# Optimization experiments

Measured on AMD Instinct MI355X. Metric: run time of the kernel, lower is better.

Reference implementation:

```python
import jax, jax.numpy as jnp
import numpy as np

NUM_EMBEDDINGS = 1024
EMBEDDING_DIM = 64
COMMITMENT_COST = 0.25
N_TOKENS = 131072


def setup_inputs() -> dict:
    key = jax.random.key(0)
    k_in, k_emb = jax.random.split(key)
    inputs = jax.random.normal(k_in, (N_TOKENS, EMBEDDING_DIM), dtype=jnp.float32)
    # torch init: uniform(-1/K, 1/K)
    codebook = jax.random.uniform(
        k_emb, (NUM_EMBEDDINGS, EMBEDDING_DIM), dtype=jnp.float32,
        minval=-1.0 / NUM_EMBEDDINGS, maxval=1.0 / NUM_EMBEDDINGS)
    return {"inputs": inputs, "codebook": codebook}


def reference(inputs, codebook):
    sg = jax.lax.stop_gradient
    distances = (jnp.sum(inputs * inputs, axis=1, keepdims=True)
                 - 2.0 * jnp.matmul(inputs, codebook.T)
                 + jnp.sum(codebook * codebook, axis=1)[None, :])
    encoding_indices = jnp.argmin(distances, axis=1)          # [N]
    # direct gather (same math as one-hot @ codebook)
    quantized = jnp.take(codebook, encoding_indices, axis=0)  # [N, D]
    # original computes e_latent_loss and q_latent_loss identically
    # (both mse(inputs, quantized.detach())), so loss = (1 + beta) * mse
    mse = jnp.mean((sg(quantized) - inputs) ** 2)
    loss = mse + COMMITMENT_COST * mse
    # straight-through estimator
    quantized_st = inputs + sg(quantized - inputs)
    # perplexity from code usage histogram (== mean of one-hot encodings)
    counts = jax.ops.segment_sum(
        jnp.ones((inputs.shape[0],), dtype=jnp.float32),
        encoding_indices, num_segments=NUM_EMBEDDINGS)
    avg_probs = counts / inputs.shape[0]
    perplexity = jnp.exp(-jnp.sum(avg_probs * jnp.log(avg_probs + 1e-10)))
    return loss, quantized_st, perplexity, encoding_indices[:, None]
```

## Files before the change

kernel.cpp:

```cpp
#include <hip/hip_runtime.h>
#include <math.h>

#define NTOK 131072
#define KC   1024
#define DIMV 64
#define NWAVE 16
#define TPW  32
#define TPB  (NWAVE * TPW)
#define CMAX 128
#define EPS  2e-3f

#define OUT_LOSS 0
#define OUT_Q    1
#define OUT_PERP (1 + NTOK * DIMV)
#define OUT_IDX  (2 + NTOK * DIMV)

#define WS_HIST 1
#define WS_NORM 1025
#define WS_PACK_BYTES 12288
#define WS_NEED (WS_PACK_BYTES + KC * DIMV * 2)

typedef __attribute__((ext_vector_type(8))) short short8;
typedef __attribute__((ext_vector_type(4))) float f32x4;

__device__ __forceinline__ float sumsq64_np(const float v[DIMV]) {
#pragma clang fp contract(off)
  {
    float r[8];
#pragma unroll
    for (int j = 0; j < 8; ++j) r[j] = v[j] * v[j];
#pragma unroll
    for (int i = 8; i < 64; i += 8) {
#pragma unroll
      for (int j = 0; j < 8; ++j) r[j] += v[i + j] * v[i + j];
    }
    return ((r[0] + r[1]) + (r[2] + r[3])) + ((r[4] + r[5]) + (r[6] + r[7]));
  }
}

__device__ __forceinline__ unsigned short bf16rne(float f) {
  unsigned int u = __float_as_uint(f);
  return (unsigned short)((u + 0x7fffu + ((u >> 16) & 1u)) >> 16);
}

__global__ void __launch_bounds__(256)
vq_pack_kernel(const float* __restrict__ cb, float* __restrict__ ws) {
  const int e = blockIdx.x * 256 + threadIdx.x;
  const int tile = e >> 7, f = (e >> 6) & 1, l = e & 63;
  const int code = tile * 16 + (l & 15);
  const int kb = f * 32 + (l >> 4) * 8;
  const float4* src = reinterpret_cast<const float4*>(cb + code * DIMV + kb);
  float4 v0 = src[0], v1 = src[1];
  float v[8] = {v0.x, v0.y, v0.z, v0.w, v1.x, v1.y, v1.z, v1.w};
  unsigned int hw[4];
#pragma unroll
  for (int j = 0; j < 4; ++j) {
    hw[j] = (unsigned int)bf16rne(v[2 * j]) |
            ((unsigned int)bf16rne(v[2 * j + 1]) << 16);
  }
  char* pack = (char*)ws + WS_PACK_BYTES;
  *(uint4*)(pack + tile * 2048 + f * 1024 + l * 16) =
      make_uint4(hw[0], hw[1], hw[2], hw[3]);
  if (e < KC) {
    float row[DIMV];
    const float4* r4 = reinterpret_cast<const float4*>(cb + e * DIMV);
#pragma unroll
    for (int i = 0; i < 16; ++i) {
      float4 t = r4[i];
      row[4 * i + 0] = t.x; row[4 * i + 1] = t.y;
      row[4 * i + 2] = t.z; row[4 * i + 3] = t.w;
    }
    ws[WS_NORM + e] = sumsq64_np(row);
  }
}

__global__ void __launch_bounds__(1024, 4)
vq_main_mfma(const float* __restrict__ xin, const float* __restrict__ cb,
             float* __restrict__ out, float* __restrict__ ws) {
  __shared__ __align__(16) char s_pack[131072];
  __shared__ float s_norm[KC];
  __shared__ unsigned int s_hist[KC];
  __shared__ unsigned int s_cand[NWAVE][CMAX];
  __shared__ unsigned long long s_key[NWAVE][TPW];
  __shared__ int s_cnt[NWAVE];

  const int tid = threadIdx.x;
  const int l   = tid & 63;
  const int wv  = tid >> 6;
  const int cls = l & 15;
  const int g   = l >> 4;
  const int blk = blockIdx.x;
  const int tb  = blk * TPB + wv * TPW;

  float* ws_mse = ws;
  unsigned int* ws_hist = (unsigned int*)ws + WS_HIST;
  const float* ws_norm = ws + WS_NORM;
  const char* pack = (const char*)ws + WS_PACK_BYTES;

  {
    const uint4* src = (const uint4*)pack;
    uint4* dst = (uint4*)s_pack;
#pragma unroll
    for (int i = 0; i < 8; ++i) dst[tid + i * 1024] = src[tid + i * 1024];
  }
  s_norm[tid] = ws_norm[tid];
  s_hist[tid] = 0u;
  if (tid < NWAVE * TPW) s_key[tid >> 5][tid & 31] = ~0ull;
  if (tid < NWAVE) s_cnt[tid] = 0;
  __syncthreads();

  short8 af[2][2];
#pragma unroll
  for (int grp = 0; grp < 2; ++grp) {
    const float* xr = xin + (size_t)(tb + grp * 16 + cls) * DIMV + g * 8;
#pragma unroll
    for (int kc = 0; kc < 2; ++kc) {
      float4 v0 = *(const float4*)(xr + kc * 32);
      float4 v1 = *(const float4*)(xr + kc * 32 + 4);
      float vv[8] = {v0.x, v0.y, v0.z, v0.w, v1.x, v1.y, v1.z, v1.w};
#pragma unroll
      for (int j = 0; j < 8; ++j) af[grp][kc][j] = (short)bf16rne(vv[j]);
    }
  }

  float minv[2][4];
#pragma unroll
  for (int grp = 0; grp < 2; ++grp)
#pragma unroll
    for (int j = 0; j < 4; ++j) minv[grp][j] = INFINITY;

#pragma unroll 1
  for (int t = 0; t < 64; ++t) {
    const char* bp = s_pack + t * 2048;
    short8 b0 = *(const short8*)(bp + l * 16);
    short8 b1 = *(const short8*)(bp + 1024 + l * 16);
    float nr = s_norm[t * 16 + cls];
#pragma unroll
    for (int grp = 0; grp < 2; ++grp) {
      f32x4 acc = {0.0f, 0.0f, 0.0f, 0.0f};
      acc = __builtin_amdgcn_mfma_f32_16x16x32_bf16(af[grp][0], b0, acc, 0, 0, 0);
      acc = __builtin_amdgcn_mfma_f32_16x16x32_bf16(af[grp][1], b1, acc, 0, 0, 0);
#pragma unroll
      for (int j = 0; j < 4; ++j)
        minv[grp][j] = fminf(minv[grp][j], fmaf(-2.0f, acc[j], nr));
    }
  }
#pragma unroll
  for (int mask = 1; mask < 16; mask <<= 1) {
#pragma unroll
    for (int grp = 0; grp < 2; ++grp)
#pragma unroll
      for (int j = 0; j < 4; ++j)
        minv[grp][j] = fminf(minv[grp][j], __shfl_xor(minv[grp][j], mask, 64));
  }
  float thr[2][4];
#pragma unroll
  for (int grp = 0; grp < 2; ++grp)
#pragma unroll
    for (int j = 0; j < 4; ++j) thr[grp][j] = minv[grp][j] + EPS;

#pragma unroll 1
  for (int t = 0; t < 64; ++t) {
    const char* bp = s_pack + t * 2048;
    short8 b0 = *(const short8*)(bp + l * 16);
    short8 b1 = *(const short8*)(bp + 1024 + l * 16);
    float nr = s_norm[t * 16 + cls];
#pragma unroll
    for (int grp = 0; grp < 2; ++grp) {
      f32x4 acc = {0.0f, 0.0f, 0.0f, 0.0f};
      acc = __builtin_amdgcn_mfma_f32_16x16x32_bf16(af[grp][0], b0, acc, 0, 0, 0);
      acc = __builtin_amdgcn_mfma_f32_16x16x32_bf16(af[grp][1], b1, acc, 0, 0, 0);
#pragma unroll
      for (int j = 0; j < 4; ++j) {
        float sv = fmaf(-2.0f, acc[j], nr);
        if (sv <= thr[grp][j]) {
          int pos = atomicAdd(&s_cnt[wv], 1);
          if (pos < CMAX)
            s_cand[wv][pos] =
                ((unsigned int)(grp * 16 + g * 4 + j) << 10) |
                (unsigned int)(t * 16 + cls);
        }
      }
    }
  }
  asm volatile("s_waitcnt lgkmcnt(0)" ::: "memory");
  const int cnt = s_cnt[wv];
  int n = cnt < CMAX ? cnt : CMAX;

  for (int base = 0; base < n; base += 64) {
    int i = base + l;
    if (i < n) {
      unsigned int pk = s_cand[wv][i];
      int m = (int)(pk >> 10), k = (int)(pk & 1023);
      const float4* xr4 = (const float4*)(xin + (size_t)(tb + m) * DIMV);
      const float4* er4 = (const float4*)(cb + (size_t)k * DIMV);
      float r[8];
      float dot = 0.0f;
#pragma unroll
      for (int s = 0; s < 8; ++s) {
        float4 a = xr4[2 * s], b = xr4[2 * s + 1];
        float4 ea = er4[2 * s], eb = er4[2 * s + 1];
        float xv[8] = {a.x, a.y, a.z, a.w, b.x, b.y, b.z, b.w};
        float ev[8] = {ea.x, ea.y, ea.z, ea.w, eb.x, eb.y, eb.z, eb.w};
        {
#pragma clang fp contract(off)
#pragma unroll
          for (int j = 0; j < 8; ++j) {
            float sq = xv[j] * xv[j];
            r[j] = (s == 0) ? sq : (r[j] + sq);
          }
        }
#pragma unroll
        for (int j = 0; j < 8; ++j) dot = __builtin_fmaf(ev[j], xv[j], dot);
      }
      float xx = ((r[0] + r[1]) + (r[2] + r[3])) + ((r[4] + r[5]) + (r[6] + r[7]));
      float d = (xx - 2.0f * dot) + s_norm[k];
      unsigned long long key =
          ((unsigned long long)__float_as_uint(d) << 10) | (unsigned long long)k;
      atomicMin(&s_key[wv][m], key);
    }
  }

  if (cnt > CMAX) {
    if (l < TPW) {
      const int m = l;
      float xv[DIMV];
      const float4* xr4 = (const float4*)(xin + (size_t)(tb + m) * DIMV);
#pragma unroll
      for (int i = 0; i < 16; ++i) {
        float4 t4 = xr4[i];
        xv[4 * i + 0] = t4.x; xv[4 * i + 1] = t4.y;
        xv[4 * i + 2] = t4.z; xv[4 * i + 3] = t4.w;
      }
      float xx = sumsq64_np(xv);
      float bd = INFINITY; int bk = 0;
      for (int k = 0; k < KC; ++k) {
        const float* e = cb + (size_t)k * DIMV;
        float dot = 0.0f;
#pragma unroll
        for (int i = 0; i < DIMV; ++i) dot = __builtin_fmaf(e[i], xv[i], dot);
        float d = (xx - 2.0f * dot) + s_norm[k];
        if (d < bd) { bd = d; bk = k; }
      }
      s_key[wv][m] =
          ((unsigned long long)__float_as_uint(bd) << 10) | (unsigned long long)bk;
    }
  }
  asm volatile("s_waitcnt lgkmcnt(0)" ::: "memory");

  {
    const int m = l & 31, h = l >> 5;
    const int token = tb + m;
    unsigned long long key = s_key[wv][m];
    const int bk = (int)(key & 1023ull);
    if (h == 0) {
      out[OUT_IDX + token] = (float)bk;
      atomicAdd(&s_hist[bk], 1u);
    }
    const float4* q4 = (const float4*)(cb + (size_t)bk * DIMV + h * 32);
    const float4* x4 = (const float4*)(xin + (size_t)token * DIMV + h * 32);
    float* oq = out + OUT_Q + (size_t)token * DIMV + h * 32;
    float mse_part = 0.0f;
#pragma unroll
    for (int rr = 0; rr < 8; ++rr) {
      float4 qv = q4[rr], xv = x4[rr];
      float d0 = qv.x - xv.x, d1 = qv.y - xv.y;
      float d2 = qv.z - xv.z, d3 = qv.w - xv.w;
      float4 o;
      o.x = xv.x + d0; o.y = xv.y + d1; o.z = xv.z + d2; o.w = xv.w + d3;
      mse_part = __builtin_fmaf(d0, d0, mse_part);
      mse_part = __builtin_fmaf(d1, d1, mse_part);
      mse_part = __builtin_fmaf(d2, d2, mse_part);
      mse_part = __builtin_fmaf(d3, d3, mse_part);
      *(float4*)(oq + 4 * rr) = o;
    }
#pragma unroll
    for (int mask = 1; mask < 64; mask <<= 1)
      mse_part += __shfl_xor(mse_part, mask, 64);
    if (l == 0) atomicAdd(ws_mse, mse_part);
  }

  __syncthreads();
  {
    unsigned int c = s_hist[tid];
    if (c) atomicAdd(&ws_hist[tid], c);
  }
}

__global__ void __launch_bounds__(256)
vq_main_valu(const float* __restrict__ xin, const float* __restrict__ cb,
             float* __restrict__ out, float* __restrict__ ws) {
  __shared__ float s_norm[KC];
  __shared__ unsigned int s_hist[KC];
  __shared__ float s_cd[256];
  __shared__ int   s_ci[256];
  const int tid = threadIdx.x;
  const int lane = tid & 63;
  const int wv = __builtin_amdgcn_readfirstlane(tid >> 6);
  float* ws_mse = ws;
  unsigned int* ws_hist = (unsigned int*)ws + WS_HIST;

  for (int k = tid; k < KC; k += 256) {
    float e[DIMV];
    const float4* e4 = reinterpret_cast<const float4*>(cb + k * DIMV);
#pragma unroll
    for (int i = 0; i < 16; ++i) {
      float4 t = e4[i];
      e[4 * i + 0] = t.x; e[4 * i + 1] = t.y;
      e[4 * i + 2] = t.z; e[4 * i + 3] = t.w;
    }
    s_norm[k] = sumsq64_np(e);
    s_hist[k] = 0u;
  }
  __syncthreads();

  const int token = blockIdx.x * 64 + lane;
  float x[DIMV];
  const float4* x4 = reinterpret_cast<const float4*>(xin + (long)token * DIMV);
#pragma unroll
  for (int i = 0; i < 16; ++i) {
    float4 t = x4[i];
    x[4 * i + 0] = t.x; x[4 * i + 1] = t.y;
    x[4 * i + 2] = t.z; x[4 * i + 3] = t.w;
  }
  float xx = sumsq64_np(x);

  float best = INFINITY;
  int bidx = 0;
#pragma unroll 1
  for (int kk = 0; kk < KC / 4; ++kk) {
    const int k = wv * (KC / 4) + kk;
    const float* e = cb + k * DIMV;
    float dot = 0.0f;
#pragma unroll
    for (int i = 0; i < DIMV; ++i) dot = __builtin_fmaf(e[i], x[i], dot);
    float d = (xx - 2.0f * dot) + s_norm[k];
    if (d < best) { best = d; bidx = k; }
  }
  s_cd[tid] = best;
  s_ci[tid] = bidx;
  __syncthreads();

  if (wv == 0) {
    float bd = s_cd[lane];
    int   bi = s_ci[lane];
#pragma unroll
    for (int w = 1; w < 4; ++w) {
      float dw = s_cd[w * 64 + lane];
      int   iw = s_ci[w * 64 + lane];
      if (dw < bd) { bd = dw; bi = iw; }
    }
    out[OUT_IDX + token] = (float)bi;
    atomicAdd(&s_hist[bi], 1u);
    const float4* q4 = (const float4*)(cb + (long)bi * DIMV);
    float acc = 0.0f;
    float4* oq4 = reinterpret_cast<float4*>(out + OUT_Q + (long)token * DIMV);
#pragma unroll
    for (int i = 0; i < 16; ++i) {
      float4 qv = q4[i];
      float d0 = qv.x - x[4 * i + 0];
      float d1 = qv.y - x[4 * i + 1];
      float d2 = qv.z - x[4 * i + 2];
      float d3 = qv.w - x[4 * i + 3];
      float4 o;
      o.x = x[4 * i + 0] + d0; o.y = x[4 * i + 1] + d1;
      o.z = x[4 * i + 2] + d2; o.w = x[4 * i + 3] + d3;
      acc = __builtin_fmaf(d0, d0, acc);
      acc = __builtin_fmaf(d1, d1, acc);
      acc = __builtin_fmaf(d2, d2, acc);
      acc = __builtin_fmaf(d3, d3, acc);
      oq4[i] = o;
    }
#pragma unroll
    for (int off = 32; off > 0; off >>= 1) acc += __shfl_down(acc, off, 64);
    if (lane == 0) atomicAdd(ws_mse, acc);
  }
  __syncthreads();
  for (int k = tid; k < KC; k += 256) {
    unsigned int c = s_hist[k];
    if (c) atomicAdd(&ws_hist[k], c);
  }
}

__global__ void __launch_bounds__(1024)
vq_final_kernel(const unsigned int* __restrict__ ws_hist,
                const float* __restrict__ ws_mse,
                float* __restrict__ out) {
  __shared__ float s_red[1024];
  const int t = threadIdx.x;
  float p = (float)ws_hist[t] / 131072.0f;
  float term = p * logf(p + 1e-10f);
  s_red[t] = term;
  __syncthreads();
#pragma unroll
  for (int s = 512; s > 0; s >>= 1) {
    if (t < s) s_red[t] += s_red[t + s];
    __syncthreads();
  }
  if (t == 0) {
    out[OUT_PERP] = expf(-s_red[0]);
    float mse = ws_mse[0] / 8388608.0f;
    out[OUT_LOSS] = mse + 0.25f * mse;
  }
}

extern "C" void kernel_launch(void* const* d_in, const int* in_sizes, int n_in,
                              void* d_out, int out_size, void* d_ws, size_t ws_size,
                              hipStream_t stream) {
  (void)in_sizes; (void)n_in; (void)out_size;
  const float* xin = (const float*)d_in[0];
  const float* cb  = (const float*)d_in[1];
  float* out = (float*)d_out;
  float* ws  = (float*)d_ws;

  hipMemsetAsync(d_ws, 0, sizeof(float) * (1 + KC), stream);
  if (ws_size >= (size_t)(WS_NEED + 256)) {
    hipLaunchKernelGGL(vq_pack_kernel, dim3(32), dim3(256), 0, stream, cb, ws);
    hipLaunchKernelGGL(vq_main_mfma, dim3(NTOK / TPB), dim3(1024), 0, stream,
                       xin, cb, out, ws);
  } else {
    hipLaunchKernelGGL(vq_main_valu, dim3(NTOK / 64), dim3(256), 0, stream,
                       xin, cb, out, ws);
  }
  hipLaunchKernelGGL(vq_final_kernel, dim3(1), dim3(1024), 0, stream,
                     (const unsigned int*)ws + WS_HIST, ws, out);
}
```

Before: 179.5 us.

## Fuse pack, main and final kernels into one MFMA kernel with last-block reduction

Merges the codebook pack, main search and final perplexity kernels into a single kernel. Each block now converts the codebook to bf16 and computes the norms directly into LDS, and the last block to finish (found with an atomic ticket) computes perplexity and loss. Block size drops to 512 threads with 64 tokens per wave (four MFMA row groups). The norm is folded into the accumulator's initial value, the B fragments are software-prefetched, and the refinement epsilon is halved. This removes two launches and the workspace round trip, at the cost of every block redundantly packing the codebook from global memory.

```diff
diff --git a/kernel.cpp b/kernel.cpp
--- a/kernel.cpp
+++ b/kernel.cpp
@@ -4,22 +4,17 @@
 #define NTOK 131072
 #define KC   1024
 #define DIMV 64
-#define NWAVE 16
-#define TPW  32
-#define TPB  (NWAVE * TPW)
-#define CMAX 128
-#define EPS  2e-3f
+#define NWAVE 8
+#define TPW  64
+#define TPB  512
+#define CMAX 256
+#define EPSH 1e-3f
 
 #define OUT_LOSS 0
 #define OUT_Q    1
 #define OUT_PERP (1 + NTOK * DIMV)
 #define OUT_IDX  (2 + NTOK * DIMV)
 
-#define WS_HIST 1
-#define WS_NORM 1025
-#define WS_PACK_BYTES 12288
-#define WS_NEED (WS_PACK_BYTES + KC * DIMV * 2)
-
 typedef __attribute__((ext_vector_type(8))) short short8;
 typedef __attribute__((ext_vector_type(4))) float f32x4;
 
@@ -43,46 +38,16 @@
   return (unsigned short)((u + 0x7fffu + ((u >> 16) & 1u)) >> 16);
 }
 
-__global__ void __launch_bounds__(256)
-vq_pack_kernel(const float* __restrict__ cb, float* __restrict__ ws) {
-  const int e = blockIdx.x * 256 + threadIdx.x;
-  const int tile = e >> 7, f = (e >> 6) & 1, l = e & 63;
-  const int code = tile * 16 + (l & 15);
-  const int kb = f * 32 + (l >> 4) * 8;
-  const float4* src = reinterpret_cast<const float4*>(cb + code * DIMV + kb);
-  float4 v0 = src[0], v1 = src[1];
-  float v[8] = {v0.x, v0.y, v0.z, v0.w, v1.x, v1.y, v1.z, v1.w};
-  unsigned int hw[4];
-#pragma unroll
-  for (int j = 0; j < 4; ++j) {
-    hw[j] = (unsigned int)bf16rne(v[2 * j]) |
-            ((unsigned int)bf16rne(v[2 * j + 1]) << 16);
-  }
-  char* pack = (char*)ws + WS_PACK_BYTES;
-  *(uint4*)(pack + tile * 2048 + f * 1024 + l * 16) =
-      make_uint4(hw[0], hw[1], hw[2], hw[3]);
-  if (e < KC) {
-    float row[DIMV];
-    const float4* r4 = reinterpret_cast<const float4*>(cb + e * DIMV);
-#pragma unroll
-    for (int i = 0; i < 16; ++i) {
-      float4 t = r4[i];
-      row[4 * i + 0] = t.x; row[4 * i + 1] = t.y;
-      row[4 * i + 2] = t.z; row[4 * i + 3] = t.w;
-    }
-    ws[WS_NORM + e] = sumsq64_np(row);
-  }
-}
-
-__global__ void __launch_bounds__(1024, 4)
-vq_main_mfma(const float* __restrict__ xin, const float* __restrict__ cb,
-             float* __restrict__ out, float* __restrict__ ws) {
+__global__ void __launch_bounds__(512)
+vq_fused(const float* __restrict__ xin, const float* __restrict__ cb,
+         float* __restrict__ out, float* __restrict__ ws) {
   __shared__ __align__(16) char s_pack[131072];
   __shared__ float s_norm[KC];
   __shared__ unsigned int s_hist[KC];
   __shared__ unsigned int s_cand[NWAVE][CMAX];
   __shared__ unsigned long long s_key[NWAVE][TPW];
   __shared__ int s_cnt[NWAVE];
+  __shared__ int s_last;
 
   const int tid = threadIdx.x;
   const int l   = tid & 63;
@@ -93,25 +58,43 @@
   const int tb  = blk * TPB + wv * TPW;
 
   float* ws_mse = ws;
-  unsigned int* ws_hist = (unsigned int*)ws + WS_HIST;
-  const float* ws_norm = ws + WS_NORM;
-  const char* pack = (const char*)ws + WS_PACK_BYTES;
-
-  {
-    const uint4* src = (const uint4*)pack;
-    uint4* dst = (uint4*)s_pack;
-#pragma unroll
-    for (int i = 0; i < 8; ++i) dst[tid + i * 1024] = src[tid + i * 1024];
-  }
-  s_norm[tid] = ws_norm[tid];
-  s_hist[tid] = 0u;
-  if (tid < NWAVE * TPW) s_key[tid >> 5][tid & 31] = ~0ull;
+  unsigned int* ws_hist = (unsigned int*)ws + 1;
+  unsigned int* ws_done = (unsigned int*)ws + 1 + KC;
+
+  for (int c = tid; c < 8192; c += 512) {
+    const int tile = c >> 7, f = (c >> 6) & 1, cl = c & 63;
+    const int code = tile * 16 + (cl & 15);
+    const int kb = f * 32 + (cl >> 4) * 8;
+    const float4* src = (const float4*)(cb + code * DIMV + kb);
+    float4 v0 = src[0], v1 = src[1];
+    float v[8] = {v0.x, v0.y, v0.z, v0.w, v1.x, v1.y, v1.z, v1.w};
+    unsigned int hw[4];
+#pragma unroll
+    for (int j = 0; j < 4; ++j) {
+      hw[j] = (unsigned int)bf16rne(v[2 * j]) |
+              ((unsigned int)bf16rne(v[2 * j + 1]) << 16);
+    }
+    *(uint4*)(s_pack + tile * 2048 + f * 1024 + cl * 16) =
+        make_uint4(hw[0], hw[1], hw[2], hw[3]);
+  }
+  for (int k = tid; k < KC; k += 512) {
+    float row[DIMV];
+    const float4* r4 = (const float4*)(cb + (size_t)k * DIMV);
+#pragma unroll
+    for (int i = 0; i < 16; ++i) {
+      float4 t = r4[i];
+      row[4 * i + 0] = t.x; row[4 * i + 1] = t.y;
+      row[4 * i + 2] = t.z; row[4 * i + 3] = t.w;
+    }
+    s_norm[k] = sumsq64_np(row);
+    s_hist[k] = 0u;
+  }
+  s_key[wv][l] = ~0ull;
   if (tid < NWAVE) s_cnt[tid] = 0;
-  __syncthreads();
-
-  short8 af[2][2];
-#pragma unroll
-  for (int grp = 0; grp < 2; ++grp) {
+
+  short8 af[4][2];
+#pragma unroll
+  for (int grp = 0; grp < 4; ++grp) {
     const float* xr = xin + (size_t)(tb + grp * 16 + cls) * DIMV + g * 8;
 #pragma unroll
     for (int kc = 0; kc < 2; ++kc) {
@@ -122,58 +105,82 @@
       for (int j = 0; j < 8; ++j) af[grp][kc][j] = (short)bf16rne(vv[j]);
     }
   }
-
-  float minv[2][4];
-#pragma unroll
-  for (int grp = 0; grp < 2; ++grp)
+  __syncthreads();
+
+  float minv[4][4];
+#pragma unroll
+  for (int grp = 0; grp < 4; ++grp)
 #pragma unroll
     for (int j = 0; j < 4; ++j) minv[grp][j] = INFINITY;
 
-#pragma unroll 1
-  for (int t = 0; t < 64; ++t) {
-    const char* bp = s_pack + t * 2048;
-    short8 b0 = *(const short8*)(bp + l * 16);
-    short8 b1 = *(const short8*)(bp + 1024 + l * 16);
-    float nr = s_norm[t * 16 + cls];
-#pragma unroll
-    for (int grp = 0; grp < 2; ++grp) {
-      f32x4 acc = {0.0f, 0.0f, 0.0f, 0.0f};
+  short8 b0 = *(const short8*)(s_pack + l * 16);
+  short8 b1 = *(const short8*)(s_pack + 1024 + l * 16);
+  float nr = s_norm[cls];
+#pragma unroll 2
+  for (int t = 0; t < 63; ++t) {
+    short8 c0 = b0, c1 = b1;
+    float cc = -0.5f * nr;
+    const char* bp = s_pack + (t + 1) * 2048 + l * 16;
+    b0 = *(const short8*)(bp);
+    b1 = *(const short8*)(bp + 1024);
+    nr = s_norm[(t + 1) * 16 + cls];
+#pragma unroll
+    for (int grp = 0; grp < 4; ++grp) {
+      f32x4 acc = {cc, cc, cc, cc};
+      acc = __builtin_amdgcn_mfma_f32_16x16x32_bf16(af[grp][0], c0, acc, 0, 0, 0);
+      acc = __builtin_amdgcn_mfma_f32_16x16x32_bf16(af[grp][1], c1, acc, 0, 0, 0);
+#pragma unroll
+      for (int j = 0; j < 4; ++j)
+        minv[grp][j] = fminf(minv[grp][j], -acc[j]);
+    }
+  }
+  {
+    float cc = -0.5f * nr;
+#pragma unroll
+    for (int grp = 0; grp < 4; ++grp) {
+      f32x4 acc = {cc, cc, cc, cc};
       acc = __builtin_amdgcn_mfma_f32_16x16x32_bf16(af[grp][0], b0, acc, 0, 0, 0);
       acc = __builtin_amdgcn_mfma_f32_16x16x32_bf16(af[grp][1], b1, acc, 0, 0, 0);
 #pragma unroll
       for (int j = 0; j < 4; ++j)
-        minv[grp][j] = fminf(minv[grp][j], fmaf(-2.0f, acc[j], nr));
+        minv[grp][j] = fminf(minv[grp][j], -acc[j]);
     }
   }
 #pragma unroll
   for (int mask = 1; mask < 16; mask <<= 1) {
 #pragma unroll
-    for (int grp = 0; grp < 2; ++grp)
+    for (int grp = 0; grp < 4; ++grp)
 #pragma unroll
       for (int j = 0; j < 4; ++j)
         minv[grp][j] = fminf(minv[grp][j], __shfl_xor(minv[grp][j], mask, 64));
   }
-  float thr[2][4];
-#pragma unroll
-  for (int grp = 0; grp < 2; ++grp)
-#pragma unroll
-    for (int j = 0; j < 4; ++j) thr[grp][j] = minv[grp][j] + EPS;
-
-#pragma unroll 1
+  float thr[4][4];
+#pragma unroll
+  for (int grp = 0; grp < 4; ++grp)
+#pragma unroll
+    for (int j = 0; j < 4; ++j) thr[grp][j] = minv[grp][j] + EPSH;
+
+  b0 = *(const short8*)(s_pack + l * 16);
+  b1 = *(const short8*)(s_pack + 1024 + l * 16);
+  nr = s_norm[cls];
+#pragma unroll 2
   for (int t = 0; t < 64; ++t) {
-    const char* bp = s_pack + t * 2048;
-    short8 b0 = *(const short8*)(bp + l * 16);
-    short8 b1 = *(const short8*)(bp + 1024 + l * 16);
-    float nr = s_norm[t * 16 + cls];
-#pragma unroll
-    for (int grp = 0; grp < 2; ++grp) {
-      f32x4 acc = {0.0f, 0.0f, 0.0f, 0.0f};
-      acc = __builtin_amdgcn_mfma_f32_16x16x32_bf16(af[grp][0], b0, acc, 0, 0, 0);
-      acc = __builtin_amdgcn_mfma_f32_16x16x32_bf16(af[grp][1], b1, acc, 0, 0, 0);
+    short8 c0 = b0, c1 = b1;
+    float cc = -0.5f * nr;
+    if (t < 63) {
+      const char* bp = s_pack + (t + 1) * 2048 + l * 16;
+      b0 = *(const short8*)(bp);
+      b1 = *(const short8*)(bp + 1024);
+      nr = s_norm[(t + 1) * 16 + cls];
+    }
+#pragma unroll
+    for (int grp = 0; grp < 4; ++grp) {
+      f32x4 acc = {cc, cc, cc, cc};
+      acc = __builtin_amdgcn_mfma_f32_16x16x32_bf16(af[grp][0], c0, acc, 0, 0, 0);
+      acc = __builtin_amdgcn_mfma_f32_16x16x32_bf16(af[grp][1], c1, acc, 0, 0, 0);
 #pragma unroll
       for (int j = 0; j < 4; ++j) {
-        float sv = fmaf(-2.0f, acc[j], nr);
-        if (sv <= thr[grp][j]) {
+        if (-acc[j] <= thr[grp][j]) {
           int pos = atomicAdd(&s_cnt[wv], 1);
           if (pos < CMAX)
             s_cand[wv][pos] =
@@ -222,47 +229,43 @@
   }
 
   if (cnt > CMAX) {
-    if (l < TPW) {
-      const int m = l;
-      float xv[DIMV];
-      const float4* xr4 = (const float4*)(xin + (size_t)(tb + m) * DIMV);
-#pragma unroll
-      for (int i = 0; i < 16; ++i) {
-        float4 t4 = xr4[i];
-        xv[4 * i + 0] = t4.x; xv[4 * i + 1] = t4.y;
-        xv[4 * i + 2] = t4.z; xv[4 * i + 3] = t4.w;
-      }
-      float xx = sumsq64_np(xv);
-      float bd = INFINITY; int bk = 0;
-      for (int k = 0; k < KC; ++k) {
-        const float* e = cb + (size_t)k * DIMV;
-        float dot = 0.0f;
-#pragma unroll
-        for (int i = 0; i < DIMV; ++i) dot = __builtin_fmaf(e[i], xv[i], dot);
-        float d = (xx - 2.0f * dot) + s_norm[k];
-        if (d < bd) { bd = d; bk = k; }
-      }
-      s_key[wv][m] =
-          ((unsigned long long)__float_as_uint(bd) << 10) | (unsigned long long)bk;
-    }
+    asm volatile("s_waitcnt lgkmcnt(0)" ::: "memory");
+    const int m = l;
+    float xv[DIMV];
+    const float4* xr4 = (const float4*)(xin + (size_t)(tb + m) * DIMV);
+#pragma unroll
+    for (int i = 0; i < 16; ++i) {
+      float4 t4 = xr4[i];
+      xv[4 * i + 0] = t4.x; xv[4 * i + 1] = t4.y;
+      xv[4 * i + 2] = t4.z; xv[4 * i + 3] = t4.w;
+    }
+    float xx = sumsq64_np(xv);
+    float bd = INFINITY; int bk = 0;
+    for (int k = 0; k < KC; ++k) {
+      const float* e = cb + (size_t)k * DIMV;
+      float dot = 0.0f;
+#pragma unroll
+      for (int i = 0; i < DIMV; ++i) dot = __builtin_fmaf(e[i], xv[i], dot);
+      float d = (xx - 2.0f * dot) + s_norm[k];
+      if (d < bd) { bd = d; bk = k; }
+    }
+    s_key[wv][m] =
+        ((unsigned long long)__float_as_uint(bd) << 10) | (unsigned long long)bk;
   }
   asm volatile("s_waitcnt lgkmcnt(0)" ::: "memory");
 
   {
-    const int m = l & 31, h = l >> 5;
-    const int token = tb + m;
-    unsigned long long key = s_key[wv][m];
+    const int token = tb + l;
+    unsigned long long key = s_key[wv][l];
     const int bk = (int)(key & 1023ull);
-    if (h == 0) {
-      out[OUT_IDX + token] = (float)bk;
-      atomicAdd(&s_hist[bk], 1u);
-    }
-    const float4* q4 = (const float4*)(cb + (size_t)bk * DIMV + h * 32);
-    const float4* x4 = (const float4*)(xin + (size_t)token * DIMV + h * 32);
-    float* oq = out + OUT_Q + (size_t)token * DIMV + h * 32;
+    out[OUT_IDX + token] = (float)bk;
+    atomicAdd(&s_hist[bk], 1u);
+    const float4* q4 = (const float4*)(cb + (size_t)bk * DIMV);
+    const float4* x4 = (const float4*)(xin + (size_t)token * DIMV);
+    float* oq = out + OUT_Q + (size_t)token * DIMV;
     float mse_part = 0.0f;
 #pragma unroll
-    for (int rr = 0; rr < 8; ++rr) {
+    for (int rr = 0; rr < 16; ++rr) {
       float4 qv = q4[rr], xv = x4[rr];
       float d0 = qv.x - xv.x, d1 = qv.y - xv.y;
       float d2 = qv.z - xv.z, d3 = qv.w - xv.w;
@@ -281,147 +284,51 @@
   }
 
   __syncthreads();
-  {
-    unsigned int c = s_hist[tid];
-    if (c) atomicAdd(&ws_hist[tid], c);
-  }
-}
-
-__global__ void __launch_bounds__(256)
-vq_main_valu(const float* __restrict__ xin, const float* __restrict__ cb,
-             float* __restrict__ out, float* __restrict__ ws) {
-  __shared__ float s_norm[KC];
-  __shared__ unsigned int s_hist[KC];
-  __shared__ float s_cd[256];
-  __shared__ int   s_ci[256];
-  const int tid = threadIdx.x;
-  const int lane = tid & 63;
-  const int wv = __builtin_amdgcn_readfirstlane(tid >> 6);
-  float* ws_mse = ws;
-  unsigned int* ws_hist = (unsigned int*)ws + WS_HIST;
-
-  for (int k = tid; k < KC; k += 256) {
-    float e[DIMV];
-    const float4* e4 = reinterpret_cast<const float4*>(cb + k * DIMV);
-#pragma unroll
-    for (int i = 0; i < 16; ++i) {
-      float4 t = e4[i];
-      e[4 * i + 0] = t.x; e[4 * i + 1] = t.y;
-      e[4 * i + 2] = t.z; e[4 * i + 3] = t.w;
-    }
-    s_norm[k] = sumsq64_np(e);
-    s_hist[k] = 0u;
-  }
-  __syncthreads();
-
-  const int token = blockIdx.x * 64 + lane;
-  float x[DIMV];
-  const float4* x4 = reinterpret_cast<const float4*>(xin + (long)token * DIMV);
-#pragma unroll
-  for (int i = 0; i < 16; ++i) {
-    float4 t = x4[i];
-    x[4 * i + 0] = t.x; x[4 * i + 1] = t.y;
-    x[4 * i + 2] = t.z; x[4 * i + 3] = t.w;
-  }
-  float xx = sumsq64_np(x);
-
-  float best = INFINITY;
-  int bidx = 0;
-#pragma unroll 1
-  for (int kk = 0; kk < KC / 4; ++kk) {
-    const int k = wv * (KC / 4) + kk;
-    const float* e = cb + k * DIMV;
-    float dot = 0.0f;
-#pragma unroll
-    for (int i = 0; i < DIMV; ++i) dot = __builtin_fmaf(e[i], x[i], dot);
-    float d = (xx - 2.0f * dot) + s_norm[k];
-    if (d < best) { best = d; bidx = k; }
-  }
-  s_cd[tid] = best;
-  s_ci[tid] = bidx;
-  __syncthreads();
-
-  if (wv == 0) {
-    float bd = s_cd[lane];
-    int   bi = s_ci[lane];
-#pragma unroll
-    for (int w = 1; w < 4; ++w) {
-      float dw = s_cd[w * 64 + lane];
-      int   iw = s_ci[w * 64 + lane];
-      if (dw < bd) { bd = dw; bi = iw; }
-    }
-    out[OUT_IDX + token] = (float)bi;
-    atomicAdd(&s_hist[bi], 1u);
-    const float4* q4 = (const float4*)(cb + (long)bi * DIMV);
-    float acc = 0.0f;
-    float4* oq4 = reinterpret_cast<float4*>(out + OUT_Q + (long)token * DIMV);
-#pragma unroll
-    for (int i = 0; i < 16; ++i) {
-      float4 qv = q4[i];
-      float d0 = qv.x - x[4 * i + 0];
-      float d1 = qv.y - x[4 * i + 1];
-      float d2 = qv.z - x[4 * i + 2];
-      float d3 = qv.w - x[4 * i + 3];
-      float4 o;
-      o.x = x[4 * i + 0] + d0; o.y = x[4 * i + 1] + d1;
-      o.z = x[4 * i + 2] + d2; o.w = x[4 * i + 3] + d3;
-      acc = __builtin_fmaf(d0, d0, acc);
-      acc = __builtin_fmaf(d1, d1, acc);
-      acc = __builtin_fmaf(d2, d2, acc);
-      acc = __builtin_fmaf(d3, d3, acc);
-      oq4[i] = o;
-    }
-#pragma unroll
-    for (int off = 32; off > 0; off >>= 1) acc += __shfl_down(acc, off, 64);
-    if (lane == 0) atomicAdd(ws_mse, acc);
-  }
-  __syncthreads();
-  for (int k = tid; k < KC; k += 256) {
+  for (int k = tid; k < KC; k += 512) {
     unsigned int c = s_hist[k];
     if (c) atomicAdd(&ws_hist[k], c);
   }
-}
-
-__global__ void __launch_bounds__(1024)
-vq_final_kernel(const unsigned int* __restrict__ ws_hist,
-                const float* __restrict__ ws_mse,
-                float* __restrict__ out) {
-  __shared__ float s_red[1024];
-  const int t = threadIdx.x;
-  float p = (float)ws_hist[t] / 131072.0f;
-  float term = p * logf(p + 1e-10f);
-  s_red[t] = term;
   __syncthreads();
-#pragma unroll
-  for (int s = 512; s > 0; s >>= 1) {
-    if (t < s) s_red[t] += s_red[t + s];
+
+  if (tid == 0) {
+    __threadfence();
+    unsigned int tkt = atomicAdd(ws_done, 1u);
+    s_last = (tkt == (unsigned int)(gridDim.x - 1)) ? 1 : 0;
+  }
+  __syncthreads();
+  if (s_last) {
+    __threadfence();
+    float term = 0.0f;
+    for (int k = tid; k < KC; k += 512) {
+      unsigned int c = atomicAdd(&ws_hist[k], 0u);
+      float p = (float)c / 131072.0f;
+      term += p * logf(p + 1e-10f);
+    }
+    s_norm[tid] = term;
     __syncthreads();
-  }
-  if (t == 0) {
-    out[OUT_PERP] = expf(-s_red[0]);
-    float mse = ws_mse[0] / 8388608.0f;
-    out[OUT_LOSS] = mse + 0.25f * mse;
+#pragma unroll
+    for (int s = 256; s > 0; s >>= 1) {
+      if (tid < s) s_norm[tid] += s_norm[tid + s];
+      __syncthreads();
+    }
+    if (tid == 0) {
+      out[OUT_PERP] = expf(-s_norm[0]);
+      float mse = atomicAdd(ws_mse, 0.0f) / 8388608.0f;
+      out[OUT_LOSS] = mse + 0.25f * mse;
+    }
   }
 }
 
 extern "C" void kernel_launch(void* const* d_in, const int* in_sizes, int n_in,
                               void* d_out, int out_size, void* d_ws, size_t ws_size,
                               hipStream_t stream) {
-  (void)in_sizes; (void)n_in; (void)out_size;
+  (void)in_sizes; (void)n_in; (void)out_size; (void)ws_size;
   const float* xin = (const float*)d_in[0];
   const float* cb  = (const float*)d_in[1];
   float* out = (float*)d_out;
   float* ws  = (float*)d_ws;
 
-  hipMemsetAsync(d_ws, 0, sizeof(float) * (1 + KC), stream);
-  if (ws_size >= (size_t)(WS_NEED + 256)) {
-    hipLaunchKernelGGL(vq_pack_kernel, dim3(32), dim3(256), 0, stream, cb, ws);
-    hipLaunchKernelGGL(vq_main_mfma, dim3(NTOK / TPB), dim3(1024), 0, stream,
-                       xin, cb, out, ws);
-  } else {
-    hipLaunchKernelGGL(vq_main_valu, dim3(NTOK / 64), dim3(256), 0, stream,
-                       xin, cb, out, ws);
-  }
-  hipLaunchKernelGGL(vq_final_kernel, dim3(1), dim3(1024), 0, stream,
-                     (const unsigned int*)ws + WS_HIST, ws, out);
+  hipMemsetAsync(d_ws, 0, sizeof(float) * (1 + KC + 1), stream);
+  hipLaunchKernelGGL(vq_fused, dim3(NTOK / TPB), dim3(512), 0, stream,
+                     xin, cb, out, ws);
 }
```

New measurement: 203.7 us. 13.5% more time.
